# Kernel optimization log

Measured on AMD Instinct MI355X. Metric: run time of the kernel, lower is better.

The kernel has to match this reference:

```python
import jax, jax.numpy as jnp
import numpy as np

FEAT = 512
N_SUPPORT = 4096
N_QUERY = 8192
N_CLASSES = 64
K = 3


def lstm_cell(x, h, c, W_ih, W_hh, b):
    # PyTorch LSTMCell: gates = x@W_ih.T + h@W_hh.T + b, order (i, f, g, o)
    g = x @ W_ih.T + h @ W_hh.T + b
    i, f, gt, o = jnp.split(g, 4, axis=-1)
    c_new = jax.nn.sigmoid(f) * c + jax.nn.sigmoid(i) * jnp.tanh(gt)
    h_new = jax.nn.sigmoid(o) * jnp.tanh(c_new)
    return h_new, c_new


def lstm_seq(xs, W_ih, W_hh, b):
    # unidirectional LSTM over a [n, feat] sequence (batch=1 squeezed)
    D = W_hh.shape[1]
    def step(carry, x):
        h, c = lstm_cell(x, carry[0], carry[1], W_ih, W_hh, b)
        return (h, c), h
    init = (jnp.zeros((D,), xs.dtype), jnp.zeros((D,), xs.dtype))
    _, hs = jax.lax.scan(step, init, xs)
    return hs


def setup_inputs() -> dict:
    key = jax.random.key(0)
    ks = jax.random.split(key, 10)
    scale = 0.04  # ~ 1/sqrt(feat_dim), PyTorch-style uniform init scale
    S = jax.random.normal(ks[0], (N_SUPPORT, FEAT), jnp.float32)
    f = jax.random.normal(ks[1], (N_QUERY, FEAT), jnp.float32)
    labels = jax.random.randint(ks[2], (N_SUPPORT,), 0, N_CLASSES)
    Y_S = jax.nn.one_hot(labels, N_CLASSES, dtype=jnp.float32)
    # bidirectional G_encoder LSTM (1 layer), combined bias b = b_ih + b_hh
    Wf_ih = jax.random.normal(ks[3], (4 * FEAT, FEAT), jnp.float32) * scale
    Wf_hh = jax.random.normal(ks[4], (4 * FEAT, FEAT), jnp.float32) * scale
    bf = jnp.zeros((4 * FEAT,), jnp.float32)
    Wb_ih = jax.random.normal(ks[5], (4 * FEAT, FEAT), jnp.float32) * scale
    Wb_hh = jax.random.normal(ks[6], (4 * FEAT, FEAT), jnp.float32) * scale
    bb = jnp.zeros((4 * FEAT,), jnp.float32)
    # FCE LSTMCell: input feat*2 -> hidden feat
    Wc_ih = jax.random.normal(ks[7], (4 * FEAT, 2 * FEAT), jnp.float32) * scale
    Wc_hh = jax.random.normal(ks[8], (4 * FEAT, FEAT), jnp.float32) * scale
    bc = jnp.zeros((4 * FEAT,), jnp.float32)
    return {"S": S, "f": f, "Y_S": Y_S,
            "Wf_ih": Wf_ih, "Wf_hh": Wf_hh, "bf": bf,
            "Wb_ih": Wb_ih, "Wb_hh": Wb_hh, "bb": bb,
            "Wc_ih": Wc_ih, "Wc_hh": Wc_hh, "bc": bc}


def reference(S, f, Y_S, Wf_ih, Wf_hh, bf, Wb_ih, Wb_hh, bb, Wc_ih, Wc_hh, bc):
    # encode_training_set: bidirectional LSTM + skip connection
    hs_fwd = lstm_seq(S, Wf_ih, Wf_hh, bf)                 # [n_s, D]
    hs_bwd = lstm_seq(S[::-1], Wb_ih, Wb_hh, bb)[::-1]     # [n_s, D]
    G = S + hs_fwd + hs_bwd
    G_norm = jnp.sqrt(jnp.sum(G * G, axis=1, keepdims=True))
    G_normalized = G / (G_norm + 1e-5)

    # FullyContextualEmbedding: K steps of attention-read + LSTMCell + residual
    h = f
    c = jnp.zeros_like(f)
    for _ in range(K):
        logit_a = h @ G.T                                   # [n_q, n_s]
        a = jax.nn.softmax(logit_a, axis=0)                 # dim=0 as in original
        r = a @ G                                           # [n_q, D]
        x = jnp.concatenate((f, r), axis=1)                 # [n_q, 2D]
        h, c = lstm_cell(x, h, c, Wc_ih, Wc_hh, bc)
        h = h + f

    scores = h @ G_normalized.T                             # [n_q, n_s]
    logprobs = jnp.log(jax.nn.softmax(scores, axis=0) @ Y_S)  # [n_q, n_classes]
    return logprobs
```

## Files before the change

### kernel.cpp

```cpp
#include <hip/hip_runtime.h>
#include <math.h>

#define FEAT 512
#define NS   4096
#define NQ   8192
#define NC   64
#define G4   2048
#define SLAB 512
#define SENT 1.0e30f

using bf16x8 = __attribute__((ext_vector_type(8))) short;
using f32x4  = __attribute__((ext_vector_type(4))) float;

__device__ __forceinline__ float sigf(float x) { return 1.0f / (1.0f + expf(-x)); }

__device__ __forceinline__ void split_bf16(float x, unsigned short& hi, unsigned short& lo) {
    unsigned u = __float_as_uint(x);
    unsigned r = u + 0x7FFFu + ((u >> 16) & 1u);
    hi = (unsigned short)(r >> 16);
    float res = x - __uint_as_float((unsigned)hi << 16);
    unsigned u2 = __float_as_uint(res);
    unsigned r2 = u2 + 0x7FFFu + ((u2 >> 16) & 1u);
    lo = (unsigned short)(r2 >> 16);
}

__global__ void kcopy(float* __restrict__ dst, const float* __restrict__ src, int n) {
    int i = blockIdx.x * blockDim.x + threadIdx.x;
    int st = gridDim.x * blockDim.x;
    for (; i < n; i += st) dst[i] = src[i];
}

__global__ void kzero(float* __restrict__ dst, int n) {
    int i = blockIdx.x * blockDim.x + threadIdx.x;
    int st = gridDim.x * blockDim.x;
    for (; i < n; i += st) dst[i] = 0.0f;
}

__global__ void kfill(float* __restrict__ dst, float v, int n) {
    int i = blockIdx.x * blockDim.x + threadIdx.x;
    int st = gridDim.x * blockDim.x;
    for (; i < n; i += st) dst[i] = v;
}

__global__ void klog(float* __restrict__ o, int n) {
    int i = blockIdx.x * blockDim.x + threadIdx.x;
    int st = gridDim.x * blockDim.x;
    for (; i < n; i += st) o[i] = logf(o[i]);
}

__global__ void pack_w(float* __restrict__ Wpack, float* __restrict__ bpack,
                       const float* __restrict__ Wc_ih, const float* __restrict__ Wc_hh,
                       const float* __restrict__ bc) {
    int i = blockIdx.x * blockDim.x + threadIdx.x;
    int st = gridDim.x * blockDim.x;
    const int n = G4 * 1536;
    for (; i < n; i += st) {
        int R = i / 1536, j = i - R * 1536;
        int k = R >> 2, g = R & 3;
        int row2 = g * FEAT + k;
        Wpack[i] = (j < 1024) ? Wc_ih[(size_t)row2 * 1024 + j]
                              : Wc_hh[(size_t)row2 * FEAT + (j - 1024)];
        if (j == 0) bpack[R] = bc[row2];
    }
}

template<int BIAS, int TRISRC>
__global__ __launch_bounds__(256)
void mm_abt(const float* __restrict__ A0, const float* __restrict__ A1,
            const float* __restrict__ A2, const float* __restrict__ B,
            int lda, int ldb, float* __restrict__ C, int ldc,
            const float* __restrict__ bias, int K)
{
    __shared__ unsigned short Ah[128][40], Al[128][40], Bh[128][40], Bl[128][40];
    const int tid = threadIdx.x;
    const int row0 = blockIdx.y * 128, col0 = blockIdx.x * 128;
    const int l = tid & 63;
    const int wm = ((tid >> 6) >> 1) * 64, wn = ((tid >> 6) & 1) * 64;
    const int fr = l & 15, fk = (l >> 4) * 8;

    f32x4 acc[4][4];
#pragma unroll
    for (int mt = 0; mt < 4; ++mt)
#pragma unroll
        for (int nt = 0; nt < 4; ++nt) acc[mt][nt] = (f32x4){0.f, 0.f, 0.f, 0.f};

    for (int k0 = 0; k0 < K; k0 += 32) {
#pragma unroll
        for (int p = 0; p < 4; ++p) {
            int flat = p * 256 + tid;
            int ar = flat >> 3, aq = (flat & 7) * 4;
            int gk = k0 + aq;
            const float* src;
            if (TRISRC) {
                int row = row0 + ar;
                src = (gk < 512)  ? (A0 + (size_t)row * FEAT + gk)
                    : (gk < 1024) ? (A1 + (size_t)row * FEAT + (gk - 512))
                                  : (A2 + (size_t)row * FEAT + (gk - 1024));
            } else {
                src = A0 + (size_t)(row0 + ar) * lda + gk;
            }
            float4 v = *(const float4*)src;
            unsigned short h0,h1,h2,h3,q0,q1,q2,q3;
            split_bf16(v.x, h0, q0); split_bf16(v.y, h1, q1);
            split_bf16(v.z, h2, q2); split_bf16(v.w, h3, q3);
            *(short4*)&Ah[ar][aq] = make_short4((short)h0,(short)h1,(short)h2,(short)h3);
            *(short4*)&Al[ar][aq] = make_short4((short)q0,(short)q1,(short)q2,(short)q3);
        }
#pragma unroll
        for (int p = 0; p < 4; ++p) {
            int flat = p * 256 + tid;
            int br = flat >> 3, bq = (flat & 7) * 4;
            float4 v = *(const float4*)(B + (size_t)(col0 + br) * ldb + k0 + bq);
            unsigned short h0,h1,h2,h3,q0,q1,q2,q3;
            split_bf16(v.x, h0, q0); split_bf16(v.y, h1, q1);
            split_bf16(v.z, h2, q2); split_bf16(v.w, h3, q3);
            *(short4*)&Bh[br][bq] = make_short4((short)h0,(short)h1,(short)h2,(short)h3);
            *(short4*)&Bl[br][bq] = make_short4((short)q0,(short)q1,(short)q2,(short)q3);
        }
        __syncthreads();

        bf16x8 ah[4], al4[4], bh[4], bl4[4];
#pragma unroll
        for (int mt = 0; mt < 4; ++mt) {
            ah[mt]  = *(const bf16x8*)&Ah[wm + mt * 16 + fr][fk];
            al4[mt] = *(const bf16x8*)&Al[wm + mt * 16 + fr][fk];
        }
#pragma unroll
        for (int nt = 0; nt < 4; ++nt) {
            bh[nt]  = *(const bf16x8*)&Bh[wn + nt * 16 + fr][fk];
            bl4[nt] = *(const bf16x8*)&Bl[wn + nt * 16 + fr][fk];
        }
#pragma unroll
        for (int mt = 0; mt < 4; ++mt)
#pragma unroll
            for (int nt = 0; nt < 4; ++nt) {
                acc[mt][nt] = __builtin_amdgcn_mfma_f32_16x16x32_bf16(ah[mt],  bh[nt],  acc[mt][nt], 0, 0, 0);
                acc[mt][nt] = __builtin_amdgcn_mfma_f32_16x16x32_bf16(al4[mt], bh[nt],  acc[mt][nt], 0, 0, 0);
                acc[mt][nt] = __builtin_amdgcn_mfma_f32_16x16x32_bf16(ah[mt],  bl4[nt], acc[mt][nt], 0, 0, 0);
            }
        __syncthreads();
    }
#pragma unroll
    for (int mt = 0; mt < 4; ++mt) {
        int row = row0 + wm + mt * 16 + (l >> 4) * 4;
#pragma unroll
        for (int nt = 0; nt < 4; ++nt) {
            int col = col0 + wn + nt * 16 + fr;
            float bv = BIAS ? bias[col] : 0.0f;
#pragma unroll
            for (int j = 0; j < 4; ++j)
                C[(size_t)(row + j) * ldc + col] = acc[mt][nt][j] + bv;
        }
    }
}

template<int ACC, int EXP>
__global__ __launch_bounds__(256)
void mm_ab(const float* __restrict__ A, int lda, const float* __restrict__ B,
           int ldb, float* __restrict__ C, int ldc, int K,
           const float* __restrict__ cm, const float* __restrict__ ciz)
{
    __shared__ unsigned short Ah[128][40], Al[128][40], Bh[128][40], Bl[128][40];
    const int tid = threadIdx.x;
    const int row0 = blockIdx.y * 128, col0 = blockIdx.x * 128;
    const int l = tid & 63;
    const int wm = ((tid >> 6) >> 1) * 64, wn = ((tid >> 6) & 1) * 64;
    const int fr = l & 15, fk = (l >> 4) * 8;

    f32x4 acc[4][4];
#pragma unroll
    for (int mt = 0; mt < 4; ++mt)
#pragma unroll
        for (int nt = 0; nt < 4; ++nt) acc[mt][nt] = (f32x4){0.f, 0.f, 0.f, 0.f};

    for (int k0 = 0; k0 < K; k0 += 32) {
#pragma unroll
        for (int p = 0; p < 4; ++p) {
            int flat = p * 256 + tid;
            int ar = flat >> 3, aq = (flat & 7) * 4;
            float4 v = *(const float4*)(A + (size_t)(row0 + ar) * lda + k0 + aq);
            if (EXP) {
                int kk = k0 + aq;
                v.x = expf(v.x - cm[kk + 0]) * ciz[kk + 0];
                v.y = expf(v.y - cm[kk + 1]) * ciz[kk + 1];
                v.z = expf(v.z - cm[kk + 2]) * ciz[kk + 2];
                v.w = expf(v.w - cm[kk + 3]) * ciz[kk + 3];
            }
            unsigned short h0,h1,h2,h3,q0,q1,q2,q3;
            split_bf16(v.x, h0, q0); split_bf16(v.y, h1, q1);
            split_bf16(v.z, h2, q2); split_bf16(v.w, h3, q3);
            *(short4*)&Ah[ar][aq] = make_short4((short)h0,(short)h1,(short)h2,(short)h3);
            *(short4*)&Al[ar][aq] = make_short4((short)q0,(short)q1,(short)q2,(short)q3);
        }
#pragma unroll
        for (int it = 0; it < 2; ++it) {
            int item = it * 256 + tid;
            int q  = item >> 4;
            int kp = item & 15;
            const float* s0 = B + (size_t)(k0 + 2 * kp) * ldb + col0 + q * 4;
            float4 v0 = *(const float4*)s0;
            float4 v1 = *(const float4*)(s0 + ldb);
            float a0[4] = {v0.x, v0.y, v0.z, v0.w};
            float a1[4] = {v1.x, v1.y, v1.z, v1.w};
#pragma unroll
            for (int cc = 0; cc < 4; ++cc) {
                unsigned short h0, q0, h1, q1;
                split_bf16(a0[cc], h0, q0);
                split_bf16(a1[cc], h1, q1);
                int col = q * 4 + cc;
                *(unsigned*)&Bh[col][2 * kp] = (unsigned)h0 | ((unsigned)h1 << 16);
                *(unsigned*)&Bl[col][2 * kp] = (unsigned)q0 | ((unsigned)q1 << 16);
            }
        }
        __syncthreads();

        bf16x8 ah[4], al4[4], bh[4], bl4[4];
#pragma unroll
        for (int mt = 0; mt < 4; ++mt) {
            ah[mt]  = *(const bf16x8*)&Ah[wm + mt * 16 + fr][fk];
            al4[mt] = *(const bf16x8*)&Al[wm + mt * 16 + fr][fk];
        }
#pragma unroll
        for (int nt = 0; nt < 4; ++nt) {
            bh[nt]  = *(const bf16x8*)&Bh[wn + nt * 16 + fr][fk];
            bl4[nt] = *(const bf16x8*)&Bl[wn + nt * 16 + fr][fk];
        }
#pragma unroll
        for (int mt = 0; mt < 4; ++mt)
#pragma unroll
            for (int nt = 0; nt < 4; ++nt) {
                acc[mt][nt] = __builtin_amdgcn_mfma_f32_16x16x32_bf16(ah[mt],  bh[nt],  acc[mt][nt], 0, 0, 0);
                acc[mt][nt] = __builtin_amdgcn_mfma_f32_16x16x32_bf16(al4[mt], bh[nt],  acc[mt][nt], 0, 0, 0);
                acc[mt][nt] = __builtin_amdgcn_mfma_f32_16x16x32_bf16(ah[mt],  bl4[nt], acc[mt][nt], 0, 0, 0);
            }
        __syncthreads();
    }
#pragma unroll
    for (int mt = 0; mt < 4; ++mt) {
        int row = row0 + wm + mt * 16 + (l >> 4) * 4;
#pragma unroll
        for (int nt = 0; nt < 4; ++nt) {
            int col = col0 + wn + nt * 16 + fr;
#pragma unroll
            for (int j = 0; j < 4; ++j) {
                size_t idx = (size_t)(row + j) * ldc + col;
                if (ACC) C[idx] += acc[mt][nt][j];
                else     C[idx]  = acc[mt][nt][j];
            }
        }
    }
}

template<int ACC, int EXP>
__global__ __launch_bounds__(256)
void gemm_ab(const float* __restrict__ A, int lda,
             const float* __restrict__ B, int ldb,
             float* __restrict__ C, int ldc, int K,
             const float* __restrict__ cm, const float* __restrict__ ciz)
{
    __shared__ float As[16][128];
    __shared__ float Bs[16][64];
    const int row0 = blockIdx.y * 128;
    const int col0 = blockIdx.x * 64;
    const int tid = threadIdx.x;
    const int tr = tid >> 4, tc = tid & 15;
    float acc[8][4];
#pragma unroll
    for (int i = 0; i < 8; ++i)
#pragma unroll
        for (int j = 0; j < 4; ++j) acc[i][j] = 0.0f;

    for (int k0 = 0; k0 < K; k0 += 16) {
#pragma unroll
        for (int p = tid; p < 512; p += 256) {
            int r = p >> 2, kq = (p & 3) * 4;
            float4 av = *(const float4*)(A + (size_t)(row0 + r) * lda + k0 + kq);
            if (EXP) {
                int kk = k0 + kq;
                av.x = expf(av.x - cm[kk + 0]) * ciz[kk + 0];
                av.y = expf(av.y - cm[kk + 1]) * ciz[kk + 1];
                av.z = expf(av.z - cm[kk + 2]) * ciz[kk + 2];
                av.w = expf(av.w - cm[kk + 3]) * ciz[kk + 3];
            }
            As[kq + 0][r] = av.x; As[kq + 1][r] = av.y; As[kq + 2][r] = av.z; As[kq + 3][r] = av.w;
        }
        {
            int kr = tid >> 4, cq = (tid & 15) * 4;
            float4 bv = *(const float4*)(B + (size_t)(k0 + kr) * ldb + col0 + cq);
            *(float4*)&Bs[kr][cq] = bv;
        }
        __syncthreads();
#pragma unroll
        for (int kk = 0; kk < 16; ++kk) {
            float4 a0 = *(const float4*)&As[kk][tr * 8];
            float4 a1 = *(const float4*)&As[kk][tr * 8 + 4];
            float4 b0 = *(const float4*)&Bs[kk][tc * 4];
            float a[8] = {a0.x, a0.y, a0.z, a0.w, a1.x, a1.y, a1.z, a1.w};
            float b[4] = {b0.x, b0.y, b0.z, b0.w};
#pragma unroll
            for (int i = 0; i < 8; ++i)
#pragma unroll
                for (int j = 0; j < 4; ++j) acc[i][j] += a[i] * b[j];
        }
        __syncthreads();
    }
#pragma unroll
    for (int i = 0; i < 8; ++i) {
        size_t idx = (size_t)(row0 + tr * 8 + i) * ldc + col0 + tc * 4;
#pragma unroll
        for (int j = 0; j < 4; ++j) {
            if (ACC) C[idx + j] += acc[i][j];
            else     C[idx + j]  = acc[i][j];
        }
    }
}

__global__ __launch_bounds__(256, 1)
void lstm_persist(const float* __restrict__ Xf, const float* __restrict__ Xb,
                  const float* __restrict__ Wf, const float* __restrict__ Wb,
                  float* __restrict__ Hf, float* __restrict__ Hb)
{
    __shared__ float hs[2][FEAT];

    const int bid = blockIdx.x;
    const int dir = bid >> 5;
    const int blk = bid & 31;
    const int tid = threadIdx.x;
    const float* W = dir ? Wb : Wf;
    const float* X = dir ? Xb : Xf;
    float* H = dir ? Hb : Hf;

    const int e = tid >> 4, l = tid & 15;
    const int hidx = blk * 16 + e;

    float4 wr[32];
#pragma unroll
    for (int g = 0; g < 4; ++g)
#pragma unroll
        for (int j = 0; j < 8; ++j)
            wr[g * 8 + j] = *(const float4*)(W + (size_t)(g * FEAT + hidx) * FEAT + l * 4 + j * 64);
#pragma unroll
    for (int i = 0; i < 32; ++i)
        asm volatile("" : "+v"(wr[i].x), "+v"(wr[i].y), "+v"(wr[i].z), "+v"(wr[i].w));

    float c_reg = 0.0f;

    for (int t = 0; t < NS; ++t) {
        const int trow = dir ? (NS - 1 - t) : t;
        const float* Xrow = X + (size_t)trow * G4;
        float x0 = 0.f, x1 = 0.f, x2 = 0.f, x3 = 0.f;
        if (l == 0) {
            x0 = Xrow[hidx];            x1 = Xrow[FEAT + hidx];
            x2 = Xrow[2 * FEAT + hidx]; x3 = Xrow[3 * FEAT + hidx];
        }
        float* hcur = hs[t & 1];
        if (t > 0) {
            const int prow = dir ? (trow + 1) : (trow - 1);
            const float* Hp = H + (size_t)prow * FEAT;
            float v0, v1;
            do {
                v0 = __hip_atomic_load(Hp + tid,       __ATOMIC_RELAXED, __HIP_MEMORY_SCOPE_AGENT);
                v1 = __hip_atomic_load(Hp + tid + 256, __ATOMIC_RELAXED, __HIP_MEMORY_SCOPE_AGENT);
            } while (v0 == SENT || v1 == SENT);
            hcur[tid] = v0; hcur[tid + 256] = v1;
        } else {
            hcur[tid] = 0.0f; hcur[tid + 256] = 0.0f;
        }
        __syncthreads();

        float4 hv4[8];
#pragma unroll
        for (int j = 0; j < 8; ++j) hv4[j] = *(const float4*)&hcur[l * 4 + j * 64];

        float dots[4];
#pragma unroll
        for (int g = 0; g < 4; ++g) {
            float s = 0.0f;
#pragma unroll
            for (int j = 0; j < 8; ++j) {
                float4 w4 = wr[g * 8 + j];
                float4 h4 = hv4[j];
                s += w4.x * h4.x + w4.y * h4.y + w4.z * h4.z + w4.w * h4.w;
            }
#pragma unroll
            for (int off = 8; off >= 1; off >>= 1) s += __shfl_xor(s, off, 64);
            dots[g] = s;
        }
        if (l == 0) {
            float gi = dots[0] + x0, gf = dots[1] + x1;
            float gg = dots[2] + x2, go = dots[3] + x3;
            float cn = sigf(gf) * c_reg + sigf(gi) * tanhf(gg);
            float hv = sigf(go) * tanhf(cn);
            c_reg = cn;
            __hip_atomic_store(H + (size_t)trow * FEAT + hidx, hv,
                               __ATOMIC_RELAXED, __HIP_MEMORY_SCOPE_AGENT);
        }
    }
}

__global__ __launch_bounds__(256)
void gnorm_fuse(const float* __restrict__ S, const float* __restrict__ Hf,
                const float* __restrict__ Hb, float* __restrict__ G,
                float* __restrict__ Gn)
{
    const int row = blockIdx.x;
    const size_t base = (size_t)row * FEAT;
    const int tid = threadIdx.x;
    float v0 = S[base + tid]       + Hf[base + tid]       + Hb[base + tid];
    float v1 = S[base + tid + 256] + Hf[base + tid + 256] + Hb[base + tid + 256];
    G[base + tid] = v0;
    G[base + tid + 256] = v1;
    float s = v0 * v0 + v1 * v1;
#pragma unroll
    for (int off = 32; off >= 1; off >>= 1) s += __shfl_xor(s, off, 64);
    __shared__ float red[4];
    if ((tid & 63) == 0) red[tid >> 6] = s;
    __syncthreads();
    float tot = red[0] + red[1] + red[2] + red[3];
    float inv = 1.0f / (sqrtf(tot) + 1e-5f);
    Gn[base + tid] = v0 * inv;
    Gn[base + tid + 256] = v1 * inv;
}

__global__ __launch_bounds__(256)
void colstats_partial(const float* __restrict__ A, float* __restrict__ pm,
                      float* __restrict__ pz)
{
    const int col = blockIdx.x * 256 + threadIdx.x;
    const int r0 = blockIdx.y * 128;
    float m = -3.0e38f, z = 0.0f;
    for (int r = 0; r < 128; ++r) {
        float v = A[(size_t)(r0 + r) * SLAB + col];
        if (v > m) { z = z * expf(m - v) + 1.0f; m = v; }
        else       { z += expf(v - m); }
    }
    pm[(size_t)blockIdx.y * SLAB + col] = m;
    pz[(size_t)blockIdx.y * SLAB + col] = z;
}

__global__ __launch_bounds__(256)
void colstats_combine(const float* __restrict__ pm, const float* __restrict__ pz,
                      float* __restrict__ cm, float* __restrict__ ciz)
{
    const int col = blockIdx.x * 256 + threadIdx.x;
    float m = -3.0e38f;
    for (int p = 0; p < 64; ++p) m = fmaxf(m, pm[(size_t)p * SLAB + col]);
    float z = 0.0f;
    for (int p = 0; p < 64; ++p) z += pz[(size_t)p * SLAB + col] * expf(pm[(size_t)p * SLAB + col] - m);
    cm[col] = m;
    ciz[col] = 1.0f / z;
}

__global__ void cell_slice(const float* __restrict__ gslab, float* __restrict__ cst,
                           float* __restrict__ hnext, const float* __restrict__ f,
                           int k0)
{
    int i = blockIdx.x * blockDim.x + threadIdx.x;
    const int st = gridDim.x * blockDim.x;
    const int n = NQ * 128;
    for (; i < n; i += st) {
        int q = i >> 7, kk = i & 127;
        float4 g = *(const float4*)(gslab + (size_t)q * 512 + kk * 4);
        int idx = q * FEAT + k0 + kk;
        float cold = cst[idx];
        float cn = sigf(g.y) * cold + sigf(g.x) * tanhf(g.z);
        float hn = sigf(g.w) * tanhf(cn) + f[idx];
        cst[idx] = cn;
        hnext[idx] = hn;
    }
}

extern "C" void kernel_launch(void* const* d_in, const int* in_sizes, int n_in,
                              void* d_out, int out_size, void* d_ws, size_t ws_size,
                              hipStream_t stream)
{
    (void)in_sizes; (void)n_in; (void)out_size; (void)ws_size;
    const float* S     = (const float*)d_in[0];
    const float* f     = (const float*)d_in[1];
    const float* Y     = (const float*)d_in[2];
    const float* Wf_ih = (const float*)d_in[3];
    const float* Wf_hh = (const float*)d_in[4];
    const float* bf    = (const float*)d_in[5];
    const float* Wb_ih = (const float*)d_in[6];
    const float* Wb_hh = (const float*)d_in[7];
    const float* bb    = (const float*)d_in[8];
    const float* Wc_ih = (const float*)d_in[9];
    const float* Wc_hh = (const float*)d_in[10];
    const float* bc    = (const float*)d_in[11];
    float* out = (float*)d_out;

    float* ws = (float*)d_ws;
    float* Xf   = ws;
    float* Xb   = ws + (size_t)8 * 1024 * 1024;
    float* r    = ws;
    float* h0   = ws + (size_t)4 * 1024 * 1024;
    float* h1   = ws + (size_t)8 * 1024 * 1024;
    float* cst  = ws + (size_t)12 * 1024 * 1024;
    size_t off  = (size_t)16 * 1024 * 1024;
    auto alloc = [&](size_t n) { float* p = ws + off; off += n; return p; };
    float* Pslab = alloc((size_t)NQ * SLAB);
    float* G     = alloc((size_t)NS * FEAT);
    float* Gn    = alloc((size_t)NS * FEAT);
    float* Wpack = alloc((size_t)G4 * 1536);
    float* bpack = alloc(G4);
    float* pm    = alloc((size_t)64 * SLAB);
    float* pz    = alloc((size_t)64 * SLAB);
    float* cm    = alloc(SLAB);
    float* ciz   = alloc(SLAB);

    float* Hf = Pslab;
    float* Hb = Pslab + (size_t)2 * 1024 * 1024;

    const dim3 B256(256);

    mm_abt<1,0><<<dim3(16, 32), B256, 0, stream>>>(S, nullptr, nullptr, Wf_ih, FEAT, FEAT, Xf, G4, bf, FEAT);
    mm_abt<1,0><<<dim3(16, 32), B256, 0, stream>>>(S, nullptr, nullptr, Wb_ih, FEAT, FEAT, Xb, G4, bb, FEAT);

    kfill<<<dim3(2048), B256, 0, stream>>>(Pslab, SENT, 4 * 1024 * 1024);
    lstm_persist<<<dim3(64), B256, 0, stream>>>(Xf, Xb, Wf_hh, Wb_hh, Hf, Hb);
    gnorm_fuse<<<dim3(NS), B256, 0, stream>>>(S, Hf, Hb, G, Gn);

    pack_w<<<dim3(2048), B256, 0, stream>>>(Wpack, bpack, Wc_ih, Wc_hh, bc);
    kcopy<<<dim3(1024), B256, 0, stream>>>(h0, f, NQ * FEAT);
    kzero<<<dim3(1024), B256, 0, stream>>>(cst, NQ * FEAT);

    for (int it = 0; it < 3; ++it) {
        float* hc = (it & 1) ? h1 : h0;
        float* hx = (it & 1) ? h0 : h1;
        for (int sb = 0; sb < NS / SLAB; ++sb) {
            const float* Gs = G + (size_t)sb * SLAB * FEAT;
            mm_abt<0,0><<<dim3(4, 64), B256, 0, stream>>>(hc, nullptr, nullptr, Gs, FEAT, FEAT, Pslab, SLAB, nullptr, FEAT);
            colstats_partial<<<dim3(2, 64), B256, 0, stream>>>(Pslab, pm, pz);
            colstats_combine<<<dim3(2), B256, 0, stream>>>(pm, pz, cm, ciz);
            if (sb == 0) mm_ab<0,1><<<dim3(4, 64), B256, 0, stream>>>(Pslab, SLAB, Gs, FEAT, r, FEAT, SLAB, cm, ciz);
            else         mm_ab<1,1><<<dim3(4, 64), B256, 0, stream>>>(Pslab, SLAB, Gs, FEAT, r, FEAT, SLAB, cm, ciz);
        }
        for (int sl = 0; sl < 4; ++sl) {
            mm_abt<1,1><<<dim3(4, 64), B256, 0, stream>>>(f, r, hc,
                Wpack + (size_t)sl * 512 * 1536, FEAT, 1536, Pslab, 512, bpack + sl * 512, 1536);
            cell_slice<<<dim3(1024), B256, 0, stream>>>(Pslab, cst, hx, f, sl * 128);
        }
    }

    for (int sb = 0; sb < NS / SLAB; ++sb) {
        const float* Gs = Gn + (size_t)sb * SLAB * FEAT;
        mm_abt<0,0><<<dim3(4, 64), B256, 0, stream>>>(h1, nullptr, nullptr, Gs, FEAT, FEAT, Pslab, SLAB, nullptr, FEAT);
        colstats_partial<<<dim3(2, 64), B256, 0, stream>>>(Pslab, pm, pz);
        colstats_combine<<<dim3(2), B256, 0, stream>>>(pm, pz, cm, ciz);
        if (sb == 0) gemm_ab<0,1><<<dim3(1, 64), B256, 0, stream>>>(Pslab, SLAB, Y + (size_t)sb * SLAB * NC, NC, out, NC, SLAB, cm, ciz);
        else         gemm_ab<1,1><<<dim3(1, 64), B256, 0, stream>>>(Pslab, SLAB, Y + (size_t)sb * SLAB * NC, NC, out, NC, SLAB, cm, ciz);
    }
    klog<<<dim3(512), B256, 0, stream>>>(out, NQ * NC);
}
```

Baseline: 15.58 ms.

## Pre-split G and FCE weights to bf16 hi/lo; widen LSTM recurrence grid

```diff
diff --git a/kernel.cpp b/kernel.cpp
--- a/kernel.cpp
+++ b/kernel.cpp
@@ -48,7 +48,8 @@
     for (; i < n; i += st) o[i] = logf(o[i]);
 }
 
-__global__ void pack_w(float* __restrict__ Wpack, float* __restrict__ bpack,
+__global__ void pack_w(unsigned short* __restrict__ Wph, unsigned short* __restrict__ Wpl,
+                       float* __restrict__ bpack,
                        const float* __restrict__ Wc_ih, const float* __restrict__ Wc_hh,
                        const float* __restrict__ bc) {
     int i = blockIdx.x * blockDim.x + threadIdx.x;
@@ -58,20 +59,103 @@
         int R = i / 1536, j = i - R * 1536;
         int k = R >> 2, g = R & 3;
         int row2 = g * FEAT + k;
-        Wpack[i] = (j < 1024) ? Wc_ih[(size_t)row2 * 1024 + j]
-                              : Wc_hh[(size_t)row2 * FEAT + (j - 1024)];
+        float v = (j < 1024) ? Wc_ih[(size_t)row2 * 1024 + j]
+                             : Wc_hh[(size_t)row2 * FEAT + (j - 1024)];
+        unsigned short h, l;
+        split_bf16(v, h, l);
+        Wph[i] = h; Wpl[i] = l;
         if (j == 0) bpack[R] = bc[row2];
+    }
+}
+
+template<int BIAS>
+__global__ __launch_bounds__(256)
+void mm_abt_f32(const float* __restrict__ A0, const float* __restrict__ B,
+                int lda, int ldb, float* __restrict__ C, int ldc,
+                const float* __restrict__ bias, int K)
+{
+    __shared__ unsigned short Ah[128][40], Al[128][40], Bh[128][40], Bl[128][40];
+    const int tid = threadIdx.x;
+    const int row0 = blockIdx.y * 128, col0 = blockIdx.x * 128;
+    const int l = tid & 63;
+    const int wm = ((tid >> 6) >> 1) * 64, wn = ((tid >> 6) & 1) * 64;
+    const int fr = l & 15, fk = (l >> 4) * 8;
+
+    f32x4 acc[4][4];
+#pragma unroll
+    for (int mt = 0; mt < 4; ++mt)
+#pragma unroll
+        for (int nt = 0; nt < 4; ++nt) acc[mt][nt] = (f32x4){0.f, 0.f, 0.f, 0.f};
+
+    for (int k0 = 0; k0 < K; k0 += 32) {
+#pragma unroll
+        for (int p = 0; p < 4; ++p) {
+            int flat = p * 256 + tid;
+            int ar = flat >> 3, aq = (flat & 7) * 4;
+            float4 v = *(const float4*)(A0 + (size_t)(row0 + ar) * lda + k0 + aq);
+            unsigned short h0,h1,h2,h3,q0,q1,q2,q3;
+            split_bf16(v.x, h0, q0); split_bf16(v.y, h1, q1);
+            split_bf16(v.z, h2, q2); split_bf16(v.w, h3, q3);
+            *(short4*)&Ah[ar][aq] = make_short4((short)h0,(short)h1,(short)h2,(short)h3);
+            *(short4*)&Al[ar][aq] = make_short4((short)q0,(short)q1,(short)q2,(short)q3);
+        }
+#pragma unroll
+        for (int p = 0; p < 4; ++p) {
+            int flat = p * 256 + tid;
+            int br = flat >> 3, bq = (flat & 7) * 4;
+            float4 v = *(const float4*)(B + (size_t)(col0 + br) * ldb + k0 + bq);
+            unsigned short h0,h1,h2,h3,q0,q1,q2,q3;
+            split_bf16(v.x, h0, q0); split_bf16(v.y, h1, q1);
+            split_bf16(v.z, h2, q2); split_bf16(v.w, h3, q3);
+            *(short4*)&Bh[br][bq] = make_short4((short)h0,(short)h1,(short)h2,(short)h3);
+            *(short4*)&Bl[br][bq] = make_short4((short)q0,(short)q1,(short)q2,(short)q3);
+        }
+        __syncthreads();
+
+        bf16x8 ah[4], al4[4], bh[4], bl4[4];
+#pragma unroll
+        for (int mt = 0; mt < 4; ++mt) {
+            ah[mt]  = *(const bf16x8*)&Ah[wm + mt * 16 + fr][fk];
+            al4[mt] = *(const bf16x8*)&Al[wm + mt * 16 + fr][fk];
+        }
+#pragma unroll
+        for (int nt = 0; nt < 4; ++nt) {
+            bh[nt]  = *(const bf16x8*)&Bh[wn + nt * 16 + fr][fk];
+            bl4[nt] = *(const bf16x8*)&Bl[wn + nt * 16 + fr][fk];
+        }
+#pragma unroll
+        for (int mt = 0; mt < 4; ++mt)
+#pragma unroll
+            for (int nt = 0; nt < 4; ++nt) {
+                acc[mt][nt] = __builtin_amdgcn_mfma_f32_16x16x32_bf16(ah[mt],  bh[nt],  acc[mt][nt], 0, 0, 0);
+                acc[mt][nt] = __builtin_amdgcn_mfma_f32_16x16x32_bf16(al4[mt], bh[nt],  acc[mt][nt], 0, 0, 0);
+                acc[mt][nt] = __builtin_amdgcn_mfma_f32_16x16x32_bf16(ah[mt],  bl4[nt], acc[mt][nt], 0, 0, 0);
+            }
+        __syncthreads();
+    }
+#pragma unroll
+    for (int mt = 0; mt < 4; ++mt) {
+        int row = row0 + wm + mt * 16 + (l >> 4) * 4;
+#pragma unroll
+        for (int nt = 0; nt < 4; ++nt) {
+            int col = col0 + wn + nt * 16 + fr;
+            float bv = BIAS ? bias[col] : 0.0f;
+#pragma unroll
+            for (int j = 0; j < 4; ++j)
+                C[(size_t)(row + j) * ldc + col] = acc[mt][nt][j] + bv;
+        }
     }
 }
 
 template<int BIAS, int TRISRC>
 __global__ __launch_bounds__(256)
-void mm_abt(const float* __restrict__ A0, const float* __restrict__ A1,
-            const float* __restrict__ A2, const float* __restrict__ B,
-            int lda, int ldb, float* __restrict__ C, int ldc,
-            const float* __restrict__ bias, int K)
-{
-    __shared__ unsigned short Ah[128][40], Al[128][40], Bh[128][40], Bl[128][40];
+void mm_abt2(const float* __restrict__ A0, const float* __restrict__ A1,
+             const float* __restrict__ A2,
+             const unsigned short* __restrict__ Bh, const unsigned short* __restrict__ Bl,
+             int lda, int ldb, float* __restrict__ C, int ldc,
+             const float* __restrict__ bias, int K)
+{
+    __shared__ unsigned short Ah[128][40], Al[128][40], Bhs[128][40], Bls[128][40];
     const int tid = threadIdx.x;
     const int row0 = blockIdx.y * 128, col0 = blockIdx.x * 128;
     const int l = tid & 63;
@@ -107,15 +191,13 @@
             *(short4*)&Al[ar][aq] = make_short4((short)q0,(short)q1,(short)q2,(short)q3);
         }
 #pragma unroll
-        for (int p = 0; p < 4; ++p) {
+        for (int p = 0; p < 2; ++p) {
             int flat = p * 256 + tid;
-            int br = flat >> 3, bq = (flat & 7) * 4;
-            float4 v = *(const float4*)(B + (size_t)(col0 + br) * ldb + k0 + bq);
-            unsigned short h0,h1,h2,h3,q0,q1,q2,q3;
-            split_bf16(v.x, h0, q0); split_bf16(v.y, h1, q1);
-            split_bf16(v.z, h2, q2); split_bf16(v.w, h3, q3);
-            *(short4*)&Bh[br][bq] = make_short4((short)h0,(short)h1,(short)h2,(short)h3);
-            *(short4*)&Bl[br][bq] = make_short4((short)q0,(short)q1,(short)q2,(short)q3);
+            int br = flat >> 2, bq = (flat & 3) * 8;
+            float4 vh = *(const float4*)(Bh + (size_t)(col0 + br) * ldb + k0 + bq);
+            float4 vl = *(const float4*)(Bl + (size_t)(col0 + br) * ldb + k0 + bq);
+            *(float4*)&Bhs[br][bq] = vh;
+            *(float4*)&Bls[br][bq] = vl;
         }
         __syncthreads();
 
@@ -127,8 +209,8 @@
         }
 #pragma unroll
         for (int nt = 0; nt < 4; ++nt) {
-            bh[nt]  = *(const bf16x8*)&Bh[wn + nt * 16 + fr][fk];
-            bl4[nt] = *(const bf16x8*)&Bl[wn + nt * 16 + fr][fk];
+            bh[nt]  = *(const bf16x8*)&Bhs[wn + nt * 16 + fr][fk];
+            bl4[nt] = *(const bf16x8*)&Bls[wn + nt * 16 + fr][fk];
         }
 #pragma unroll
         for (int mt = 0; mt < 4; ++mt)
@@ -154,13 +236,14 @@
     }
 }
 
-template<int ACC, int EXP>
+template<int ACC>
 __global__ __launch_bounds__(256)
-void mm_ab(const float* __restrict__ A, int lda, const float* __restrict__ B,
-           int ldb, float* __restrict__ C, int ldc, int K,
-           const float* __restrict__ cm, const float* __restrict__ ciz)
-{
-    __shared__ unsigned short Ah[128][40], Al[128][40], Bh[128][40], Bl[128][40];
+void mm_ab2(const float* __restrict__ A, int lda,
+            const unsigned short* __restrict__ Bh, const unsigned short* __restrict__ Bl,
+            int ldb, float* __restrict__ C, int ldc, int K,
+            const float* __restrict__ cm, const float* __restrict__ ciz)
+{
+    __shared__ unsigned short Ah[128][40], Al[128][40], Bhs[128][40], Bls[128][40];
     const int tid = threadIdx.x;
     const int row0 = blockIdx.y * 128, col0 = blockIdx.x * 128;
     const int l = tid & 63;
@@ -179,13 +262,11 @@
             int flat = p * 256 + tid;
             int ar = flat >> 3, aq = (flat & 7) * 4;
             float4 v = *(const float4*)(A + (size_t)(row0 + ar) * lda + k0 + aq);
-            if (EXP) {
-                int kk = k0 + aq;
-                v.x = expf(v.x - cm[kk + 0]) * ciz[kk + 0];
-                v.y = expf(v.y - cm[kk + 1]) * ciz[kk + 1];
-                v.z = expf(v.z - cm[kk + 2]) * ciz[kk + 2];
-                v.w = expf(v.w - cm[kk + 3]) * ciz[kk + 3];
-            }
+            int kk = k0 + aq;
+            v.x = expf(v.x - cm[kk + 0]) * ciz[kk + 0];
+            v.y = expf(v.y - cm[kk + 1]) * ciz[kk + 1];
+            v.z = expf(v.z - cm[kk + 2]) * ciz[kk + 2];
+            v.w = expf(v.w - cm[kk + 3]) * ciz[kk + 3];
             unsigned short h0,h1,h2,h3,q0,q1,q2,q3;
             split_bf16(v.x, h0, q0); split_bf16(v.y, h1, q1);
             split_bf16(v.z, h2, q2); split_bf16(v.w, h3, q3);
@@ -193,23 +274,25 @@
             *(short4*)&Al[ar][aq] = make_short4((short)q0,(short)q1,(short)q2,(short)q3);
         }
 #pragma unroll
-        for (int it = 0; it < 2; ++it) {
-            int item = it * 256 + tid;
+        for (int it2 = 0; it2 < 2; ++it2) {
+            int item = it2 * 256 + tid;
             int q  = item >> 4;
             int kp = item & 15;
-            const float* s0 = B + (size_t)(k0 + 2 * kp) * ldb + col0 + q * 4;
-            float4 v0 = *(const float4*)s0;
-            float4 v1 = *(const float4*)(s0 + ldb);
-            float a0[4] = {v0.x, v0.y, v0.z, v0.w};
-            float a1[4] = {v1.x, v1.y, v1.z, v1.w};
+            const unsigned short* sh = Bh + (size_t)(k0 + 2 * kp) * ldb + col0 + q * 4;
+            const unsigned short* sl = Bl + (size_t)(k0 + 2 * kp) * ldb + col0 + q * 4;
+            ushort4 h0 = *(const ushort4*)sh;
+            ushort4 h1 = *(const ushort4*)(sh + ldb);
+            ushort4 l0 = *(const ushort4*)sl;
+            ushort4 l1 = *(const ushort4*)(sl + ldb);
+            unsigned short h0a[4] = {h0.x, h0.y, h0.z, h0.w};
+            unsigned short h1a[4] = {h1.x, h1.y, h1.z, h1.w};
+            unsigned short l0a[4] = {l0.x, l0.y, l0.z, l0.w};
+            unsigned short l1a[4] = {l1.x, l1.y, l1.z, l1.w};
 #pragma unroll
             for (int cc = 0; cc < 4; ++cc) {
-                unsigned short h0, q0, h1, q1;
-                split_bf16(a0[cc], h0, q0);
-                split_bf16(a1[cc], h1, q1);
                 int col = q * 4 + cc;
-                *(unsigned*)&Bh[col][2 * kp] = (unsigned)h0 | ((unsigned)h1 << 16);
-                *(unsigned*)&Bl[col][2 * kp] = (unsigned)q0 | ((unsigned)q1 << 16);
+                *(unsigned*)&Bhs[col][2 * kp] = (unsigned)h0a[cc] | ((unsigned)h1a[cc] << 16);
+                *(unsigned*)&Bls[col][2 * kp] = (unsigned)l0a[cc] | ((unsigned)l1a[cc] << 16);
             }
         }
         __syncthreads();
@@ -222,8 +305,8 @@
         }
 #pragma unroll
         for (int nt = 0; nt < 4; ++nt) {
-            bh[nt]  = *(const bf16x8*)&Bh[wn + nt * 16 + fr][fk];
-            bl4[nt] = *(const bf16x8*)&Bl[wn + nt * 16 + fr][fk];
+            bh[nt]  = *(const bf16x8*)&Bhs[wn + nt * 16 + fr][fk];
+            bl4[nt] = *(const bf16x8*)&Bls[wn + nt * 16 + fr][fk];
         }
 #pragma unroll
         for (int mt = 0; mt < 4; ++mt)
@@ -251,7 +334,7 @@
     }
 }
 
-template<int ACC, int EXP>
+template<int ACC>
 __global__ __launch_bounds__(256)
 void gemm_ab(const float* __restrict__ A, int lda,
              const float* __restrict__ B, int ldb,
@@ -275,13 +358,11 @@
         for (int p = tid; p < 512; p += 256) {
             int r = p >> 2, kq = (p & 3) * 4;
             float4 av = *(const float4*)(A + (size_t)(row0 + r) * lda + k0 + kq);
-            if (EXP) {
-                int kk = k0 + kq;
-                av.x = expf(av.x - cm[kk + 0]) * ciz[kk + 0];
-                av.y = expf(av.y - cm[kk + 1]) * ciz[kk + 1];
-                av.z = expf(av.z - cm[kk + 2]) * ciz[kk + 2];
-                av.w = expf(av.w - cm[kk + 3]) * ciz[kk + 3];
-            }
+            int kk = k0 + kq;
+            av.x = expf(av.x - cm[kk + 0]) * ciz[kk + 0];
+            av.y = expf(av.y - cm[kk + 1]) * ciz[kk + 1];
+            av.z = expf(av.z - cm[kk + 2]) * ciz[kk + 2];
+            av.w = expf(av.w - cm[kk + 3]) * ciz[kk + 3];
             As[kq + 0][r] = av.x; As[kq + 1][r] = av.y; As[kq + 2][r] = av.z; As[kq + 3][r] = av.w;
         }
         {
@@ -323,25 +404,28 @@
     __shared__ float hs[2][FEAT];
 
     const int bid = blockIdx.x;
-    const int dir = bid >> 5;
-    const int blk = bid & 31;
+    const int dir = bid >> 7;
+    const int blk = bid & 127;
     const int tid = threadIdx.x;
     const float* W = dir ? Wb : Wf;
     const float* X = dir ? Xb : Xf;
     float* H = dir ? Hb : Hf;
 
-    const int e = tid >> 4, l = tid & 15;
-    const int hidx = blk * 16 + e;
-
-    float4 wr[32];
+    const int e = tid >> 6;
+    const int lane = tid & 63;
+    const int hidx = blk * 4 + e;
+
+    float4 w[4][2];
 #pragma unroll
     for (int g = 0; g < 4; ++g)
 #pragma unroll
-        for (int j = 0; j < 8; ++j)
-            wr[g * 8 + j] = *(const float4*)(W + (size_t)(g * FEAT + hidx) * FEAT + l * 4 + j * 64);
-#pragma unroll
-    for (int i = 0; i < 32; ++i)
-        asm volatile("" : "+v"(wr[i].x), "+v"(wr[i].y), "+v"(wr[i].z), "+v"(wr[i].w));
+        for (int j = 0; j < 2; ++j)
+            w[g][j] = *(const float4*)(W + (size_t)(g * FEAT + hidx) * FEAT + lane * 4 + j * 256);
+#pragma unroll
+    for (int g = 0; g < 4; ++g)
+#pragma unroll
+        for (int j = 0; j < 2; ++j)
+            asm volatile("" : "+v"(w[g][j].x), "+v"(w[g][j].y), "+v"(w[g][j].z), "+v"(w[g][j].w));
 
     float c_reg = 0.0f;
 
@@ -349,7 +433,7 @@
         const int trow = dir ? (NS - 1 - t) : t;
         const float* Xrow = X + (size_t)trow * G4;
         float x0 = 0.f, x1 = 0.f, x2 = 0.f, x3 = 0.f;
-        if (l == 0) {
+        if (lane == 0) {
             x0 = Xrow[hidx];            x1 = Xrow[FEAT + hidx];
             x2 = Xrow[2 * FEAT + hidx]; x3 = Xrow[3 * FEAT + hidx];
         }
@@ -368,25 +452,19 @@
         }
         __syncthreads();
 
-        float4 hv4[8];
-#pragma unroll
-        for (int j = 0; j < 8; ++j) hv4[j] = *(const float4*)&hcur[l * 4 + j * 64];
+        float4 h0 = *(const float4*)&hcur[lane * 4];
+        float4 h1 = *(const float4*)&hcur[256 + lane * 4];
 
         float dots[4];
 #pragma unroll
         for (int g = 0; g < 4; ++g) {
-            float s = 0.0f;
-#pragma unroll
-            for (int j = 0; j < 8; ++j) {
-                float4 w4 = wr[g * 8 + j];
-                float4 h4 = hv4[j];
-                s += w4.x * h4.x + w4.y * h4.y + w4.z * h4.z + w4.w * h4.w;
-            }
-#pragma unroll
-            for (int off = 8; off >= 1; off >>= 1) s += __shfl_xor(s, off, 64);
+            float s = w[g][0].x * h0.x + w[g][0].y * h0.y + w[g][0].z * h0.z + w[g][0].w * h0.w
+                    + w[g][1].x * h1.x + w[g][1].y * h1.y + w[g][1].z * h1.z + w[g][1].w * h1.w;
+#pragma unroll
+            for (int off = 32; off >= 1; off >>= 1) s += __shfl_xor(s, off, 64);
             dots[g] = s;
         }
-        if (l == 0) {
+        if (lane == 0) {
             float gi = dots[0] + x0, gf = dots[1] + x1;
             float gg = dots[2] + x2, go = dots[3] + x3;
             float cn = sigf(gf) * c_reg + sigf(gi) * tanhf(gg);
@@ -400,16 +478,15 @@
 
 __global__ __launch_bounds__(256)
 void gnorm_fuse(const float* __restrict__ S, const float* __restrict__ Hf,
-                const float* __restrict__ Hb, float* __restrict__ G,
-                float* __restrict__ Gn)
+                const float* __restrict__ Hb,
+                unsigned short* __restrict__ Gh, unsigned short* __restrict__ Gl,
+                unsigned short* __restrict__ Gnh, unsigned short* __restrict__ Gnl)
 {
     const int row = blockIdx.x;
     const size_t base = (size_t)row * FEAT;
     const int tid = threadIdx.x;
     float v0 = S[base + tid]       + Hf[base + tid]       + Hb[base + tid];
     float v1 = S[base + tid + 256] + Hf[base + tid + 256] + Hb[base + tid + 256];
-    G[base + tid] = v0;
-    G[base + tid + 256] = v1;
     float s = v0 * v0 + v1 * v1;
 #pragma unroll
     for (int off = 32; off >= 1; off >>= 1) s += __shfl_xor(s, off, 64);
@@ -418,8 +495,11 @@
     __syncthreads();
     float tot = red[0] + red[1] + red[2] + red[3];
     float inv = 1.0f / (sqrtf(tot) + 1e-5f);
-    Gn[base + tid] = v0 * inv;
-    Gn[base + tid + 256] = v1 * inv;
+    unsigned short h, l;
+    split_bf16(v0, h, l);        Gh[base + tid] = h;        Gl[base + tid] = l;
+    split_bf16(v1, h, l);        Gh[base + tid + 256] = h;  Gl[base + tid + 256] = l;
+    split_bf16(v0 * inv, h, l);  Gnh[base + tid] = h;       Gnl[base + tid] = l;
+    split_bf16(v1 * inv, h, l);  Gnh[base + tid + 256] = h; Gnl[base + tid + 256] = l;
 }
 
 __global__ __launch_bounds__(256)
@@ -499,9 +579,12 @@
     size_t off  = (size_t)16 * 1024 * 1024;
     auto alloc = [&](size_t n) { float* p = ws + off; off += n; return p; };
     float* Pslab = alloc((size_t)NQ * SLAB);
-    float* G     = alloc((size_t)NS * FEAT);
-    float* Gn    = alloc((size_t)NS * FEAT);
-    float* Wpack = alloc((size_t)G4 * 1536);
+    unsigned short* Gh  = (unsigned short*)alloc(1024 * 1024);
+    unsigned short* Gl  = (unsigned short*)alloc(1024 * 1024);
+    unsigned short* Gnh = (unsigned short*)alloc(1024 * 1024);
+    unsigned short* Gnl = (unsigned short*)alloc(1024 * 1024);
+    unsigned short* Wph = (unsigned short*)alloc(1536 * 1024);
+    unsigned short* Wpl = (unsigned short*)alloc(1536 * 1024);
     float* bpack = alloc(G4);
     float* pm    = alloc((size_t)64 * SLAB);
     float* pz    = alloc((size_t)64 * SLAB);
@@ -513,14 +596,14 @@
 
     const dim3 B256(256);
 
-    mm_abt<1,0><<<dim3(16, 32), B256, 0, stream>>>(S, nullptr, nullptr, Wf_ih, FEAT, FEAT, Xf, G4, bf, FEAT);
-    mm_abt<1,0><<<dim3(16, 32), B256, 0, stream>>>(S, nullptr, nullptr, Wb_ih, FEAT, FEAT, Xb, G4, bb, FEAT);
+    mm_abt_f32<1><<<dim3(16, 32), B256, 0, stream>>>(S, Wf_ih, FEAT, FEAT, Xf, G4, bf, FEAT);
+    mm_abt_f32<1><<<dim3(16, 32), B256, 0, stream>>>(S, Wb_ih, FEAT, FEAT, Xb, G4, bb, FEAT);
 
     kfill<<<dim3(2048), B256, 0, stream>>>(Pslab, SENT, 4 * 1024 * 1024);
-    lstm_persist<<<dim3(64), B256, 0, stream>>>(Xf, Xb, Wf_hh, Wb_hh, Hf, Hb);
-    gnorm_fuse<<<dim3(NS), B256, 0, stream>>>(S, Hf, Hb, G, Gn);
-
-    pack_w<<<dim3(2048), B256, 0, stream>>>(Wpack, bpack, Wc_ih, Wc_hh, bc);
+    lstm_persist<<<dim3(256), B256, 0, stream>>>(Xf, Xb, Wf_hh, Wb_hh, Hf, Hb);
+    gnorm_fuse<<<dim3(NS), B256, 0, stream>>>(S, Hf, Hb, Gh, Gl, Gnh, Gnl);
+
+    pack_w<<<dim3(2048), B256, 0, stream>>>(Wph, Wpl, bpack, Wc_ih, Wc_hh, bc);
     kcopy<<<dim3(1024), B256, 0, stream>>>(h0, f, NQ * FEAT);
     kzero<<<dim3(1024), B256, 0, stream>>>(cst, NQ * FEAT);
 
@@ -528,27 +611,32 @@
         float* hc = (it & 1) ? h1 : h0;
         float* hx = (it & 1) ? h0 : h1;
         for (int sb = 0; sb < NS / SLAB; ++sb) {
-            const float* Gs = G + (size_t)sb * SLAB * FEAT;
-            mm_abt<0,0><<<dim3(4, 64), B256, 0, stream>>>(hc, nullptr, nullptr, Gs, FEAT, FEAT, Pslab, SLAB, nullptr, FEAT);
+            const unsigned short* Gsh = Gh + (size_t)sb * SLAB * FEAT;
+            const unsigned short* Gsl = Gl + (size_t)sb * SLAB * FEAT;
+            mm_abt2<0,0><<<dim3(4, 64), B256, 0, stream>>>(hc, nullptr, nullptr, Gsh, Gsl,
+                                                           FEAT, FEAT, Pslab, SLAB, nullptr, FEAT);
             colstats_partial<<<dim3(2, 64), B256, 0, stream>>>(Pslab, pm, pz);
             colstats_combine<<<dim3(2), B256, 0, stream>>>(pm, pz, cm, ciz);
-            if (sb == 0) mm_ab<0,1><<<dim3(4, 64), B256, 0, stream>>>(Pslab, SLAB, Gs, FEAT, r, FEAT, SLAB, cm, ciz);
-            else         mm_ab<1,1><<<dim3(4, 64), B256, 0, stream>>>(Pslab, SLAB, Gs, FEAT, r, FEAT, SLAB, cm, ciz);
+            if (sb == 0) mm_ab2<0><<<dim3(4, 64), B256, 0, stream>>>(Pslab, SLAB, Gsh, Gsl, FEAT, r, FEAT, SLAB, cm, ciz);
+            else         mm_ab2<1><<<dim3(4, 64), B256, 0, stream>>>(Pslab, SLAB, Gsh, Gsl, FEAT, r, FEAT, SLAB, cm, ciz);
         }
         for (int sl = 0; sl < 4; ++sl) {
-            mm_abt<1,1><<<dim3(4, 64), B256, 0, stream>>>(f, r, hc,
-                Wpack + (size_t)sl * 512 * 1536, FEAT, 1536, Pslab, 512, bpack + sl * 512, 1536);
+            mm_abt2<1,1><<<dim3(4, 64), B256, 0, stream>>>(f, r, hc,
+                Wph + (size_t)sl * 512 * 1536, Wpl + (size_t)sl * 512 * 1536,
+                FEAT, 1536, Pslab, 512, bpack + sl * 512, 1536);
             cell_slice<<<dim3(1024), B256, 0, stream>>>(Pslab, cst, hx, f, sl * 128);
         }
     }
 
     for (int sb = 0; sb < NS / SLAB; ++sb) {
-        const float* Gs = Gn + (size_t)sb * SLAB * FEAT;
-        mm_abt<0,0><<<dim3(4, 64), B256, 0, stream>>>(h1, nullptr, nullptr, Gs, FEAT, FEAT, Pslab, SLAB, nullptr, FEAT);
+        const unsigned short* Gsh = Gnh + (size_t)sb * SLAB * FEAT;
+        const unsigned short* Gsl = Gnl + (size_t)sb * SLAB * FEAT;
+        mm_abt2<0,0><<<dim3(4, 64), B256, 0, stream>>>(h1, nullptr, nullptr, Gsh, Gsl,
+                                                       FEAT, FEAT, Pslab, SLAB, nullptr, FEAT);
         colstats_partial<<<dim3(2, 64), B256, 0, stream>>>(Pslab, pm, pz);
         colstats_combine<<<dim3(2), B256, 0, stream>>>(pm, pz, cm, ciz);
-        if (sb == 0) gemm_ab<0,1><<<dim3(1, 64), B256, 0, stream>>>(Pslab, SLAB, Y + (size_t)sb * SLAB * NC, NC, out, NC, SLAB, cm, ciz);
-        else         gemm_ab<1,1><<<dim3(1, 64), B256, 0, stream>>>(Pslab, SLAB, Y + (size_t)sb * SLAB * NC, NC, out, NC, SLAB, cm, ciz);
+        if (sb == 0) gemm_ab<0><<<dim3(1, 64), B256, 0, stream>>>(Pslab, SLAB, Y + (size_t)sb * SLAB * NC, NC, out, NC, SLAB, cm, ciz);
+        else         gemm_ab<1><<<dim3(1, 64), B256, 0, stream>>>(Pslab, SLAB, Y + (size_t)sb * SLAB * NC, NC, out, NC, SLAB, cm, ciz);
     }
     klog<<<dim3(512), B256, 0, stream>>>(out, NQ * NC);
 }
```

After: 19.10 ms. +22.6%, slower.
